# Kernel tuning notes

Measured on AMD Instinct MI355X. Metric: run time of the kernel, lower is better.

Reference implementation:

```python
import jax, jax.numpy as jnp
import numpy as np

B = 512
IN_FEATURES = 512
OUT_FEATURES = 100
KERNEL_DIM = 5


def setup_inputs() -> dict:
    key = jax.random.key(0)
    kx, kT = jax.random.split(key)
    x = jax.random.normal(kx, (B, IN_FEATURES), dtype=jnp.float32)
    # nn.init.normal_(T, 0, 1)
    T = jax.random.normal(kT, (IN_FEATURES, OUT_FEATURES, KERNEL_DIM), dtype=jnp.float32)
    return {"x": x, "T": T}


def reference(x, T):
    # matrices = x @ T.view(in, out*k) -> (B, out, k)
    M = jnp.einsum('bi,iok->bok', x, T)  # [B, O, K]
    # pairwise L1 distance over kernel dim: norm[i, j, o] = sum_k |M[i,o,k] - M[j,o,k]|
    norm = jnp.abs(M[:, None, :, :] - M[None, :, :, :]).sum(-1)  # [B, B, O]
    expnorm = jnp.exp(-norm)
    # sum over first batch axis; subtract 1 to remove self-term (exp(0) = 1)
    o_b = expnorm.sum(0) - 1.0  # [B, O]
    return o_b
```

## Files before the change

kernel.cpp:

```cpp
#include <hip/hip_runtime.h>
#include <math.h>


#define NB    512
#define NIN   512
#define NOUT  100
#define KDIM  5
#define NCOL  (NOUT*KDIM)
#define KZ    8
#define MP_ELEMS (NB*NCOL)
#define M8_LD 800
#define LOG2E 1.4426950408889634f

__global__ __launch_bounds__(256) void gemm_kernel(const float* __restrict__ A,
                                                   const float* __restrict__ Bm,
                                                   float* __restrict__ Mpart) {
    __shared__ float As[64][68];
    __shared__ float Bs[64][68];

    const int tx = threadIdx.x;
    const int ty = threadIdx.y;
    const int tid = ty * 16 + tx;
    const int bn = blockIdx.x * 64;
    const int bm = blockIdx.y * 64;
    const int kz = blockIdx.z;
    const int kt = kz * 64;

    #pragma unroll
    for (int l = 0; l < 4; ++l) {
        int idx = tid + l * 256;
        int row = idx >> 4, q = idx & 15;
        float4 v = *reinterpret_cast<const float4*>(&A[(bm + row) * NIN + kt + q * 4]);
        *reinterpret_cast<float4*>(&As[row][q * 4]) = v;
    }
    #pragma unroll
    for (int l = 0; l < 4; ++l) {
        int idx = tid + l * 256;
        int row = idx >> 4, q = idx & 15;
        int col = bn + q * 4;
        float4 v;
        if (col + 3 < NCOL) {
            v = *reinterpret_cast<const float4*>(&Bm[(kt + row) * NCOL + col]);
        } else {
            v.x = (col + 0 < NCOL) ? Bm[(kt + row) * NCOL + col + 0] : 0.f;
            v.y = (col + 1 < NCOL) ? Bm[(kt + row) * NCOL + col + 1] : 0.f;
            v.z = (col + 2 < NCOL) ? Bm[(kt + row) * NCOL + col + 2] : 0.f;
            v.w = (col + 3 < NCOL) ? Bm[(kt + row) * NCOL + col + 3] : 0.f;
        }
        *reinterpret_cast<float4*>(&Bs[row][q * 4]) = v;
    }
    __syncthreads();

    float acc[4][4];
    #pragma unroll
    for (int i = 0; i < 4; ++i)
        #pragma unroll
        for (int j = 0; j < 4; ++j) acc[i][j] = 0.f;

    #pragma unroll 4
    for (int k = 0; k < 64; k += 4) {
        float4 a4[4], b4[4];
        #pragma unroll
        for (int i = 0; i < 4; ++i)
            a4[i] = *reinterpret_cast<const float4*>(&As[ty * 4 + i][k]);
        #pragma unroll
        for (int kk = 0; kk < 4; ++kk)
            b4[kk] = *reinterpret_cast<const float4*>(&Bs[k + kk][tx * 4]);
        #pragma unroll
        for (int kk = 0; kk < 4; ++kk) {
            const float* bp = reinterpret_cast<const float*>(&b4[kk]);
            #pragma unroll
            for (int i = 0; i < 4; ++i) {
                const float a = reinterpret_cast<const float*>(&a4[i])[kk];
                #pragma unroll
                for (int j = 0; j < 4; ++j) acc[i][j] += a * bp[j];
            }
        }
    }

    float* C = Mpart + kz * MP_ELEMS;
    #pragma unroll
    for (int i = 0; i < 4; ++i) {
        const int row = bm + ty * 4 + i;
        const int col0 = bn + tx * 4;
        if (col0 + 3 < NCOL) {
            float4 v = make_float4(acc[i][0], acc[i][1], acc[i][2], acc[i][3]);
            *reinterpret_cast<float4*>(&C[row * NCOL + col0]) = v;
        } else {
            #pragma unroll
            for (int j = 0; j < 4; ++j)
                if (col0 + j < NCOL) C[row * NCOL + col0 + j] = acc[i][j];
        }
    }
}

__global__ __launch_bounds__(256) void reduce_kernel(const float* __restrict__ Mpart,
                                                     float* __restrict__ M8) {
    const unsigned n = blockIdx.x * 256 + threadIdx.x;
    const float4* P = reinterpret_cast<const float4*>(Mpart);
    float4 s = P[n];
    #pragma unroll
    for (int z = 1; z < KZ; ++z) {
        float4 v = P[z * (MP_ELEMS / 4) + n];
        s.x += v.x; s.y += v.y; s.z += v.z; s.w += v.w;
    }
    const unsigned b  = n / 125;
    const unsigned c  = (n - b * 125) * 4;
    const float sv[4] = {s.x * LOG2E, s.y * LOG2E, s.z * LOG2E, s.w * LOG2E};
    #pragma unroll
    for (int e = 0; e < 4; ++e) {
        const unsigned col = c + e;
        const unsigned o   = col / KDIM;
        const unsigned kk  = col - o * KDIM;
        M8[b * M8_LD + o * 8 + kk] = sv[e];
    }
}

__global__ __launch_bounds__(256) void pairwise_kernel(const float* __restrict__ M8,
                                                       float* __restrict__ out) {
    __shared__ float Ms[NB * 8];
    __shared__ float red[64][9];

    const int o   = blockIdx.x;
    const int jc  = blockIdx.y;
    const int tid = threadIdx.x;

    {
        const int half = tid & 1;
        for (int b = tid >> 1; b < NB; b += 128) {
            const float* src = M8 + b * M8_LD + o * 8 + half * 4;
            *reinterpret_cast<float4*>(&Ms[b * 8 + half * 4]) =
                *reinterpret_cast<const float4*>(src);
        }
    }
    __syncthreads();

    const int jl = tid & 31;
    const int ig = tid >> 5;
    const int jA = jc * 64 + jl;
    const int jB = jA + 32;
    const int i0 = ig * 64;

    const float4 av = *reinterpret_cast<const float4*>(&Ms[jA * 8]);
    const float  a4 = Ms[jA * 8 + 4];
    const float4 bv = *reinterpret_cast<const float4*>(&Ms[jB * 8]);
    const float  b4 = Ms[jB * 8 + 4];

    float accA = 0.0f, accB = 0.0f;
    #pragma unroll 8
    for (int i = i0; i < i0 + 64; ++i) {
        float4 v = *reinterpret_cast<const float4*>(&Ms[i * 8]);
        float v4 = Ms[i * 8 + 4];
        float nA = fabsf(v.x - av.x) + fabsf(v.y - av.y) + fabsf(v.z - av.z)
                 + fabsf(v.w - av.w) + fabsf(v4 - a4);
        float nB = fabsf(v.x - bv.x) + fabsf(v.y - bv.y) + fabsf(v.z - bv.z)
                 + fabsf(v.w - bv.w) + fabsf(v4 - b4);
        accA += exp2f(-nA);
        accB += exp2f(-nB);
    }

    red[jl][ig]      = accA;
    red[jl + 32][ig] = accB;
    __syncthreads();

    if (tid < 64) {
        float tot = -1.0f;
        #pragma unroll
        for (int g = 0; g < 8; ++g) tot += red[tid][g];
        out[(jc * 64 + tid) * NOUT + o] = tot;
    }
}

extern "C" void kernel_launch(void* const* d_in, const int* in_sizes, int n_in,
                              void* d_out, int out_size, void* d_ws, size_t ws_size,
                              hipStream_t stream) {
    const float* x = (const float*)d_in[0];
    const float* T = (const float*)d_in[1];
    float* Mpart = (float*)d_ws;
    float* M8    = (float*)d_ws + KZ * MP_ELEMS;
    float* out   = (float*)d_out;

    gemm_kernel<<<dim3(8, 8, KZ), dim3(16, 16), 0, stream>>>(x, T, Mpart);
    reduce_kernel<<<250, 256, 0, stream>>>(Mpart, M8);
    pairwise_kernel<<<dim3(NOUT, 8), 256, 0, stream>>>(M8, out);
}
```

Baseline: 86.15 us.

## Fuse split-K reduction into pairwise kernel and remap block indices

Removes the separate reduce kernel. Each pairwise block now sums the eight split-K partial products for its output column directly from the partial buffer while loading shared memory. This saves one launch and the round trip through the intermediate M8 buffer. In exchange, every one of the 8 column-chunk blocks per output redoes the same 8-way reduction, giving 8x redundant reads of the partials through strided, uncoalesced scalar loads. The launch is a 1D grid of 832 blocks with a swizzled o/jc mapping so that blocks sharing an output column are adjacent and may reuse cache.

```diff
diff --git a/kernel.cpp b/kernel.cpp
--- a/kernel.cpp
+++ b/kernel.cpp
@@ -9,7 +9,6 @@
 #define NCOL  (NOUT*KDIM)
 #define KZ    8
 #define MP_ELEMS (NB*NCOL)
-#define M8_LD 800
 #define LOG2E 1.4426950408889634f
 
 __global__ __launch_bounds__(256) void gemm_kernel(const float* __restrict__ A,
@@ -94,44 +93,36 @@
     }
 }
 
-__global__ __launch_bounds__(256) void reduce_kernel(const float* __restrict__ Mpart,
-                                                     float* __restrict__ M8) {
-    const unsigned n = blockIdx.x * 256 + threadIdx.x;
-    const float4* P = reinterpret_cast<const float4*>(Mpart);
-    float4 s = P[n];
-    #pragma unroll
-    for (int z = 1; z < KZ; ++z) {
-        float4 v = P[z * (MP_ELEMS / 4) + n];
-        s.x += v.x; s.y += v.y; s.z += v.z; s.w += v.w;
-    }
-    const unsigned b  = n / 125;
-    const unsigned c  = (n - b * 125) * 4;
-    const float sv[4] = {s.x * LOG2E, s.y * LOG2E, s.z * LOG2E, s.w * LOG2E};
-    #pragma unroll
-    for (int e = 0; e < 4; ++e) {
-        const unsigned col = c + e;
-        const unsigned o   = col / KDIM;
-        const unsigned kk  = col - o * KDIM;
-        M8[b * M8_LD + o * 8 + kk] = sv[e];
-    }
-}
-
-__global__ __launch_bounds__(256) void pairwise_kernel(const float* __restrict__ M8,
-                                                       float* __restrict__ out) {
+__global__ __launch_bounds__(256) void pairfused_kernel(const float* __restrict__ Mpart,
+                                                        float* __restrict__ out) {
     __shared__ float Ms[NB * 8];
     __shared__ float red[64][9];
 
-    const int o   = blockIdx.x;
-    const int jc  = blockIdx.y;
+    const int wg = blockIdx.x;
+    const int o  = (wg & 7) + 8 * (wg >> 6);
+    const int jc = (wg >> 3) & 7;
+    if (o >= NOUT) return;
+
     const int tid = threadIdx.x;
 
     {
-        const int half = tid & 1;
-        for (int b = tid >> 1; b < NB; b += 128) {
-            const float* src = M8 + b * M8_LD + o * 8 + half * 4;
-            *reinterpret_cast<float4*>(&Ms[b * 8 + half * 4]) =
-                *reinterpret_cast<const float4*>(src);
+        const int b0 = tid * 2;
+        float s0[5] = {0.f, 0.f, 0.f, 0.f, 0.f};
+        float s1[5] = {0.f, 0.f, 0.f, 0.f, 0.f};
+        const float* base = Mpart + (size_t)o * KDIM + (size_t)b0 * NCOL;
+        #pragma unroll
+        for (int z = 0; z < KZ; ++z) {
+            const float* p0 = base + (size_t)z * MP_ELEMS;
+            const float* p1 = p0 + NCOL;
+            #pragma unroll
+            for (int k = 0; k < 5; ++k) s0[k] += p0[k];
+            #pragma unroll
+            for (int k = 0; k < 5; ++k) s1[k] += p1[k];
         }
+        #pragma unroll
+        for (int k = 0; k < 5; ++k) Ms[b0 * 8 + k]       = s0[k] * LOG2E;
+        #pragma unroll
+        for (int k = 0; k < 5; ++k) Ms[(b0 + 1) * 8 + k] = s1[k] * LOG2E;
     }
     __syncthreads();
 
@@ -177,10 +168,8 @@
     const float* x = (const float*)d_in[0];
     const float* T = (const float*)d_in[1];
     float* Mpart = (float*)d_ws;
-    float* M8    = (float*)d_ws + KZ * MP_ELEMS;
     float* out   = (float*)d_out;
 
     gemm_kernel<<<dim3(8, 8, KZ), dim3(16, 16), 0, stream>>>(x, T, Mpart);
-    reduce_kernel<<<250, 256, 0, stream>>>(Mpart, M8);
-    pairwise_kernel<<<dim3(NOUT, 8), 256, 0, stream>>>(M8, out);
+    pairfused_kernel<<<832, 256, 0, stream>>>(Mpart, out);
 }
```

Result: slower. 103.9 us (+20.6%).
